# Kernel tuning notes

Measured on AMD Instinct MI355X. Metric: run time of the kernel, lower is better.

## Reference

```python
import jax, jax.numpy as jnp
import numpy as np
import math

N_S = 4096
N_T = 4096
R = 0.05
SIGMA = 0.2
K = 100.0
T = 1.0
S_MAX = 300.0
B = 100.0
ALPHA_STR = 30.0
CHI = 6.0
LAMBDA_PDE = 1.0
LAMBDA_BC = 10.0
LAMBDA_TC = 10.0
HUBER_DELTA = 0.01
ALPHA = 2.0 * R / SIGMA ** 2            # 2r/sigma^2
TAU_MAX = 0.5 * SIGMA ** 2 * T
DU = 1.0 / (N_S - 1)                     # dS_norm for the S-stencils
DT_NORM = TAU_MAX / (N_T - 1)            # dt_norm for the t-stencil


def _solve_depressed_cubic(Q):
    # Faithful port of CubicStretching._solve_depressed_cubic (hyperbolic root formula).
    p = CHI
    q = CHI * Q
    sp = math.sqrt(p)
    arg = abs(q) / (2.0 * p * sp / (3.0 * math.sqrt(3.0)))
    arg = max(1.0, arg)
    c = 2.0 * sp * math.cosh(math.acosh(arg) / 3.0)
    return -c if q >= 0 else c


C1 = _solve_depressed_cubic((B - 0.0) / ALPHA_STR)
C2 = _solve_depressed_cubic((B - S_MAX) / ALPHA_STR)


def _stretch_metrics(u):
    # CubicStretching.compute_metrics: S(u), dS/du, d2S/du2.
    L = C2 * u + C1 * (1.0 - u)
    dL = C2 - C1
    S = B + ALPHA_STR * (L ** 3 / CHI + L)
    dS = ALPHA_STR * dL * (0.5 * L ** 2 + 1.0)
    d2S = ALPHA_STR * dL ** 2 * L
    return S, dS, d2S


def setup_inputs() -> dict:
    key = jax.random.key(0)
    V_norm = 0.1 * jax.random.normal(key, (1, 1, N_S, N_T), dtype=jnp.float32)
    return {"V_norm": V_norm}


def reference(V_norm):
    # u-grid along S (axis 2), t-grid along time (axis 3)
    u = jnp.linspace(0.0, 1.0, N_S, dtype=jnp.float32)[None, None, :, None]  # [1,1,N_S,1]
    t = jnp.linspace(0.0, 1.0, N_T, dtype=jnp.float32)                       # [N_T]

    S_phys, S_u, S_uu = _stretch_metrics(u)
    S_norm = S_phys / S_MAX       # stretched physical coordinate, normalized
    S_u_n = S_u / S_MAX
    S_uu_n = S_uu / S_MAX

    # FD stencils: (3,1) central diff / second diff along S, (1,3) central diff along t,
    # all with replicate padding (= torch padding_mode='replicate').
    Vp = jnp.pad(V_norm, ((0, 0), (0, 0), (1, 1), (0, 0)), mode='edge')
    V_u = (Vp[:, :, 2:, :] - Vp[:, :, :-2, :]) / (2.0 * DU)
    V_uu = (Vp[:, :, 2:, :] - 2.0 * V_norm + Vp[:, :, :-2, :]) / DU ** 2
    Vt = jnp.pad(V_norm, ((0, 0), (0, 0), (0, 0), (1, 1)), mode='edge')
    V_t = (Vt[:, :, :, 2:] - Vt[:, :, :, :-2]) / (2.0 * DT_NORM)

    # Chain rule from uniform u to stretched S
    V_S = V_u / S_u_n
    V_SS = (V_uu * S_u_n - V_u * S_uu_n) / S_u_n ** 3
    V_SS = jnp.clip(V_SS, -100.0, 100.0)

    residual = V_t - S_norm ** 2 * V_SS - ALPHA * S_norm * V_S + ALPHA * V_norm
    # interior mask = relu(1 - S0 - Smax - T - t0) == strict interior of the grid
    n_int = (N_S - 2) * (N_T - 2)
    pde_loss = jnp.sum(residual[:, :, 1:-1, 1:-1] ** 2) / n_int

    # far-field BC at S = S_max (row N_S-1): call option -> 1 - K exp(-r(1-t))/S_max
    bc_target = 1.0 - K * jnp.exp(-R * (1.0 - t)) / S_MAX
    loss_Smax = jnp.sum((V_norm[0, 0, -1, :] - bc_target) ** 2) / N_T

    # terminal condition at t = T (col N_t-1): softplus payoff on the UNIFORM u grid
    # (forward rebinds S_norm = self.S_grid_norm before calling terminal_payoff)
    payoff = jax.nn.softplus(50.0 * (u[0, 0, :, 0] - K / S_MAX)) / 50.0
    diff_T = V_norm[0, 0, :, -1] - payoff
    abs_d = jnp.abs(diff_T)
    loss_T = jnp.sum(jnp.where(abs_d < HUBER_DELTA,
                               0.5 * diff_T ** 2,
                               HUBER_DELTA * (abs_d - 0.5 * HUBER_DELTA))) / N_S

    total = LAMBDA_PDE * pde_loss + LAMBDA_BC * loss_Smax + LAMBDA_TC * loss_T
    return total
```

## Files before the change

### kernel.cpp

```cpp
#include <hip/hip_runtime.h>
#include <math.h>

#define NS 4096
#define NT 4096
#define RPB 4
#define NBLK (NS / RPB)

__device__ __forceinline__ double block_reduce(double v, int tid) {
    #pragma unroll
    for (int off = 32; off > 0; off >>= 1)
        v += __shfl_down(v, off, 64);
    __shared__ double lds[4];
    const int lane = tid & 63, wv = tid >> 6;
    if (lane == 0) lds[wv] = v;
    __syncthreads();
    return lds[0] + lds[1] + lds[2] + lds[3];
}

__device__ __forceinline__ void load16(const float* __restrict__ p, float* d) {
    const float4 x0 = *(const float4*)(p);
    const float4 x1 = *(const float4*)(p + 4);
    const float4 x2 = *(const float4*)(p + 8);
    const float4 x3 = *(const float4*)(p + 12);
    d[0]=x0.x; d[1]=x0.y; d[2]=x0.z;  d[3]=x0.w;
    d[4]=x1.x; d[5]=x1.y; d[6]=x1.z;  d[7]=x1.w;
    d[8]=x2.x; d[9]=x2.y; d[10]=x2.z; d[11]=x2.w;
    d[12]=x3.x;d[13]=x3.y;d[14]=x3.z; d[15]=x3.w;
}

__global__ __launch_bounds__(256) void bs_main(const float* __restrict__ V,
                                               double* __restrict__ part,
                                               double C1, double C2) {
    const int tid = threadIdx.x;
    const int r0  = blockIdx.x * RPB;
    const int j0  = tid * 16;

    const double DU = 1.0 / (double)(NS - 1);
    const double dL = C2 - C1;

    const float INV2DU = 2047.5f;
    const float INVDU2 = 16769025.0f;
    const float INV2DT = 102375.0f;
    const float AL     = 2.5f;

    float a[16], b[16], c[16];
    const int rm = (r0 > 0) ? r0 - 1 : 0;
    load16(V + (size_t)rm * NT + j0, a);
    load16(V + (size_t)r0 * NT + j0, b);

    double pde = 0.0, bc = 0.0, tc = 0.0;

    #pragma unroll
    for (int rr = 0; rr < RPB; ++rr) {
        const int r  = r0 + rr;
        const int rn = (r + 1 < NS) ? r + 1 : NS - 1;
        load16(V + (size_t)rn * NT + j0, c);

        const double u   = (double)r * DU;
        const double L   = C2 * u + C1 * (1.0 - u);
        const double S   = 100.0 + 30.0 * (L * L * L / 6.0 + L);
        const double dS  = 30.0 * dL * (0.5 * L * L + 1.0);
        const double d2S = 30.0 * dL * dL * L;
        const float Sn   = (float)(S   / 300.0);
        const float Sun  = (float)(dS  / 300.0);
        const float Suun = (float)(d2S / 300.0);
        const float invSun  = 1.0f / Sun;
        const float invSun3 = invSun * invSun * invSun;
        const float Sn2 = Sn * Sn;
        const float ASn = AL * Sn;

        if (r >= 1 && r <= NS - 2) {
            const float lf = (j0 > 0)       ? V[(size_t)r * NT + j0 - 1]  : 0.0f;
            const float rt = (j0 + 16 < NT) ? V[(size_t)r * NT + j0 + 16] : 0.0f;

            float pf = 0.0f;
            #pragma unroll
            for (int k = 0; k < 16; ++k) {
                const int j = j0 + k;
                if (j >= 1 && j <= NT - 2) {
                    const float cm = (k == 0)  ? lf : b[k - 1];
                    const float cp = (k == 15) ? rt : b[k + 1];
                    const float Vu  = (c[k] - a[k]) * INV2DU;
                    const float Vuu = (c[k] - 2.0f * b[k] + a[k]) * INVDU2;
                    const float Vt  = (cp - cm) * INV2DT;
                    const float VS  = Vu * invSun;
                    float VSS = (Vuu * Sun - Vu * Suun) * invSun3;
                    VSS = fminf(fmaxf(VSS, -100.0f), 100.0f);
                    const float res = Vt - Sn2 * VSS - ASn * VS + AL * b[k];
                    pf += res * res;
                }
            }
            pde += (double)pf;
        }

        if (r == NS - 1) {
            #pragma unroll
            for (int k = 0; k < 16; ++k) {
                const float t   = (float)(j0 + k) * (1.0f / (float)(NT - 1));
                const float tgt = 1.0f - (100.0f / 300.0f) * expf(-0.05f * (1.0f - t));
                const float d   = b[k] - tgt;
                bc += (double)(d * d);
            }
        }

        if (tid == 255) {
            const float ui = (float)u;
            const float x  = 50.0f * (ui - 100.0f / 300.0f);
            const float sp = fmaxf(x, 0.0f) + log1pf(expf(-fabsf(x)));
            const float payoff = sp * (1.0f / 50.0f);
            const float d  = b[15] - payoff;
            const float ad = fabsf(d);
            tc += (double)((ad < 0.01f) ? 0.5f * d * d : 0.01f * (ad - 0.005f));
        }

        #pragma unroll
        for (int k = 0; k < 16; ++k) { a[k] = b[k]; b[k] = c[k]; }
    }

    const double n_int = (double)(NS - 2) * (double)(NT - 2);
    double contrib = pde * (1.0 / n_int)
                   + bc  * (10.0 / (double)NT)
                   + tc  * (10.0 / (double)NS);

    contrib = block_reduce(contrib, tid);
    if (tid == 0) part[blockIdx.x] = contrib;
}

__global__ __launch_bounds__(256) void bs_final(const double* __restrict__ part,
                                                float* __restrict__ out) {
    const int tid = threadIdx.x;
    double s = 0.0;
    for (int idx = tid; idx < NBLK; idx += 256) s += part[idx];
    s = block_reduce(s, tid);
    if (tid == 0) out[0] = (float)s;
}

static double cubic_root_host(double Q) {
    const double p = 6.0;
    const double q = p * Q;
    const double sp = sqrt(p);
    double arg = fabs(q) / (2.0 * p * sp / (3.0 * sqrt(3.0)));
    if (arg < 1.0) arg = 1.0;
    const double c = 2.0 * sp * cosh(acosh(arg) / 3.0);
    return (q >= 0.0) ? -c : c;
}

extern "C" void kernel_launch(void* const* d_in, const int* in_sizes, int n_in,
                              void* d_out, int out_size, void* d_ws, size_t ws_size,
                              hipStream_t stream) {
    const float* V  = (const float*)d_in[0];
    float* out      = (float*)d_out;
    double* part    = (double*)d_ws;

    const double C1 = cubic_root_host((100.0 - 0.0)   / 30.0);
    const double C2 = cubic_root_host((100.0 - 300.0) / 30.0);

    bs_main <<<NBLK, 256, 0, stream>>>(V, part, C1, C2);
    bs_final<<<1,    256, 0, stream>>>(part, out);
}
```

Before: 100.2 us.

## Split columns across four blocks, preload row window, compute metrics in float

Each thread now handles 4 columns instead of 16, and the grid is split into four column chunks, giving four times as many blocks and more memory-level parallelism. All six rows and the halo values are loaded up front instead of being streamed row by row. The stretch metrics are computed in float rather than double, and the per-thread PDE sum is kept in float, which trades some precision for cheaper arithmetic. The final reduction now sums four times as many partials, and the extra blocks read the shared halo rows more often.

```diff
diff --git a/kernel.cpp b/kernel.cpp
--- a/kernel.cpp
+++ b/kernel.cpp
@@ -4,7 +4,8 @@
 #define NS 4096
 #define NT 4096
 #define RPB 4
-#define NBLK (NS / RPB)
+#define CQ  4
+#define NBLK ((NS / RPB) * CQ)
 
 __device__ __forceinline__ double block_reduce(double v, int tid) {
     #pragma unroll
@@ -17,69 +18,67 @@
     return lds[0] + lds[1] + lds[2] + lds[3];
 }
 
-__device__ __forceinline__ void load16(const float* __restrict__ p, float* d) {
-    const float4 x0 = *(const float4*)(p);
-    const float4 x1 = *(const float4*)(p + 4);
-    const float4 x2 = *(const float4*)(p + 8);
-    const float4 x3 = *(const float4*)(p + 12);
-    d[0]=x0.x; d[1]=x0.y; d[2]=x0.z;  d[3]=x0.w;
-    d[4]=x1.x; d[5]=x1.y; d[6]=x1.z;  d[7]=x1.w;
-    d[8]=x2.x; d[9]=x2.y; d[10]=x2.z; d[11]=x2.w;
-    d[12]=x3.x;d[13]=x3.y;d[14]=x3.z; d[15]=x3.w;
-}
-
-__global__ __launch_bounds__(256) void bs_main(const float* __restrict__ V,
-                                               double* __restrict__ part,
-                                               double C1, double C2) {
+__global__ __launch_bounds__(256, 6) void bs_main(const float* __restrict__ V,
+                                                  double* __restrict__ part,
+                                                  float C1, float C2) {
     const int tid = threadIdx.x;
-    const int r0  = blockIdx.x * RPB;
-    const int j0  = tid * 16;
-
-    const double DU = 1.0 / (double)(NS - 1);
-    const double dL = C2 - C1;
+    const int cb  = blockIdx.x & (CQ - 1);
+    const int rg  = blockIdx.x / CQ;
+    const int r0  = rg * RPB;
+    const int j0  = cb * (NT / CQ) + tid * 4;
 
     const float INV2DU = 2047.5f;
     const float INVDU2 = 16769025.0f;
     const float INV2DT = 102375.0f;
     const float AL     = 2.5f;
+    const float dL     = C2 - C1;
 
-    float a[16], b[16], c[16];
-    const int rm = (r0 > 0) ? r0 - 1 : 0;
-    load16(V + (size_t)rm * NT + j0, a);
-    load16(V + (size_t)r0 * NT + j0, b);
+    float w[6][4];
+    #pragma unroll
+    for (int q = 0; q < 6; ++q) {
+        int r = r0 - 1 + q;
+        r = (r < 0) ? 0 : ((r > NS - 1) ? NS - 1 : r);
+        const float4 x = *(const float4*)(V + (size_t)r * NT + j0);
+        w[q][0] = x.x; w[q][1] = x.y; w[q][2] = x.z; w[q][3] = x.w;
+    }
+    float lf[RPB], rt[RPB];
+    #pragma unroll
+    for (int rr = 0; rr < RPB; ++rr) {
+        const int r = r0 + rr;
+        lf[rr] = (j0 > 0)      ? V[(size_t)r * NT + j0 - 1] : 0.0f;
+        rt[rr] = (j0 + 4 < NT) ? V[(size_t)r * NT + j0 + 4] : 0.0f;
+    }
 
-    double pde = 0.0, bc = 0.0, tc = 0.0;
+    float pde = 0.0f;
+    double bc = 0.0, tc = 0.0;
 
     #pragma unroll
     for (int rr = 0; rr < RPB; ++rr) {
-        const int r  = r0 + rr;
-        const int rn = (r + 1 < NS) ? r + 1 : NS - 1;
-        load16(V + (size_t)rn * NT + j0, c);
+        const int r = r0 + rr;
+        const float* a = w[rr];
+        const float* b = w[rr + 1];
+        const float* c = w[rr + 2];
 
-        const double u   = (double)r * DU;
-        const double L   = C2 * u + C1 * (1.0 - u);
-        const double S   = 100.0 + 30.0 * (L * L * L / 6.0 + L);
-        const double dS  = 30.0 * dL * (0.5 * L * L + 1.0);
-        const double d2S = 30.0 * dL * dL * L;
-        const float Sn   = (float)(S   / 300.0);
-        const float Sun  = (float)(dS  / 300.0);
-        const float Suun = (float)(d2S / 300.0);
+        const float u    = (float)r * (1.0f / (float)(NS - 1));
+        const float L    = C2 * u + C1 * (1.0f - u);
+        const float S    = 100.0f + 30.0f * (L * L * L * (1.0f / 6.0f) + L);
+        const float dS   = 30.0f * dL * (0.5f * L * L + 1.0f);
+        const float d2S  = 30.0f * dL * dL * L;
+        const float Sn   = S   * (1.0f / 300.0f);
+        const float Sun  = dS  * (1.0f / 300.0f);
+        const float Suun = d2S * (1.0f / 300.0f);
         const float invSun  = 1.0f / Sun;
         const float invSun3 = invSun * invSun * invSun;
         const float Sn2 = Sn * Sn;
         const float ASn = AL * Sn;
 
         if (r >= 1 && r <= NS - 2) {
-            const float lf = (j0 > 0)       ? V[(size_t)r * NT + j0 - 1]  : 0.0f;
-            const float rt = (j0 + 16 < NT) ? V[(size_t)r * NT + j0 + 16] : 0.0f;
-
-            float pf = 0.0f;
             #pragma unroll
-            for (int k = 0; k < 16; ++k) {
+            for (int k = 0; k < 4; ++k) {
                 const int j = j0 + k;
                 if (j >= 1 && j <= NT - 2) {
-                    const float cm = (k == 0)  ? lf : b[k - 1];
-                    const float cp = (k == 15) ? rt : b[k + 1];
+                    const float cm = (k == 0) ? lf[rr] : b[k - 1];
+                    const float cp = (k == 3) ? rt[rr] : b[k + 1];
                     const float Vu  = (c[k] - a[k]) * INV2DU;
                     const float Vuu = (c[k] - 2.0f * b[k] + a[k]) * INVDU2;
                     const float Vt  = (cp - cm) * INV2DT;
@@ -87,15 +86,14 @@
                     float VSS = (Vuu * Sun - Vu * Suun) * invSun3;
                     VSS = fminf(fmaxf(VSS, -100.0f), 100.0f);
                     const float res = Vt - Sn2 * VSS - ASn * VS + AL * b[k];
-                    pf += res * res;
+                    pde += res * res;
                 }
             }
-            pde += (double)pf;
         }
 
         if (r == NS - 1) {
             #pragma unroll
-            for (int k = 0; k < 16; ++k) {
+            for (int k = 0; k < 4; ++k) {
                 const float t   = (float)(j0 + k) * (1.0f / (float)(NT - 1));
                 const float tgt = 1.0f - (100.0f / 300.0f) * expf(-0.05f * (1.0f - t));
                 const float d   = b[k] - tgt;
@@ -103,24 +101,20 @@
             }
         }
 
-        if (tid == 255) {
-            const float ui = (float)u;
-            const float x  = 50.0f * (ui - 100.0f / 300.0f);
+        if (cb == CQ - 1 && tid == 255) {
+            const float x  = 50.0f * (u - 100.0f / 300.0f);
             const float sp = fmaxf(x, 0.0f) + log1pf(expf(-fabsf(x)));
             const float payoff = sp * (1.0f / 50.0f);
-            const float d  = b[15] - payoff;
+            const float d  = b[3] - payoff;
             const float ad = fabsf(d);
             tc += (double)((ad < 0.01f) ? 0.5f * d * d : 0.01f * (ad - 0.005f));
         }
-
-        #pragma unroll
-        for (int k = 0; k < 16; ++k) { a[k] = b[k]; b[k] = c[k]; }
     }
 
     const double n_int = (double)(NS - 2) * (double)(NT - 2);
-    double contrib = pde * (1.0 / n_int)
-                   + bc  * (10.0 / (double)NT)
-                   + tc  * (10.0 / (double)NS);
+    double contrib = (double)pde * (1.0 / n_int)
+                   + bc * (10.0 / (double)NT)
+                   + tc * (10.0 / (double)NS);
 
     contrib = block_reduce(contrib, tid);
     if (tid == 0) part[blockIdx.x] = contrib;
@@ -155,6 +149,6 @@
     const double C1 = cubic_root_host((100.0 - 0.0)   / 30.0);
     const double C2 = cubic_root_host((100.0 - 300.0) / 30.0);
 
-    bs_main <<<NBLK, 256, 0, stream>>>(V, part, C1, C2);
+    bs_main <<<NBLK, 256, 0, stream>>>(V, part, (float)C1, (float)C2);
     bs_final<<<1,    256, 0, stream>>>(part, out);
 }
```

Result: no change. 100.4 us (+0.2%).
